# Kernel optimization log

Measured on AMD Instinct MI355X. Metric: run time of the kernel, lower is better.

The kernel has to match this reference:

```python
import jax, jax.numpy as jnp
import numpy as np

N_NODES = 100000
N_EDGES = 1250000
F_RAW = 48      # raw node feature dim
F_LOC = 16      # location embedding dim
F1 = 48         # filters_1
F_OUT = 64      # out_channels


def _glorot(key, shape):
    fan_in, fan_out = shape[0], shape[1]
    scale = jnp.sqrt(6.0 / (fan_in + fan_out)).astype(jnp.float32)
    return jax.random.uniform(key, shape, jnp.float32, -1.0, 1.0) * scale


def setup_inputs() -> dict:
    key = jax.random.key(0)
    k_e, k_x, k_l, k_w1, k_w2 = jax.random.split(key, 5)
    edge_indices = jax.random.randint(k_e, (2, N_EDGES), 0, N_NODES, dtype=jnp.int64)
    features = jax.random.normal(k_x, (N_NODES, F_RAW), jnp.float32)
    location_embedding = jax.random.normal(k_l, (N_NODES, F_LOC), jnp.float32)
    W1 = _glorot(k_w1, (F_RAW + F_LOC, F1))
    b1 = jnp.zeros((F1,), jnp.float32)
    W2 = _glorot(k_w2, (F1 + F_LOC, F_OUT))
    b2 = jnp.zeros((F_OUT,), jnp.float32)
    return {"edge_indices": edge_indices, "features": features,
            "location_embedding": location_embedding,
            "W1": W1, "b1": b1, "W2": W2, "b2": b2}


def gcn_conv(x, src, dst, W, b, n_nodes):
    """PyG GCNConv: add self-loops, symmetric normalization, linear + bias."""
    h = x @ W  # [N, F_out]
    # degree counts include the self-loop (+1)
    deg = jnp.zeros((n_nodes,), h.dtype).at[dst].add(1.0) + 1.0
    dinv = jax.lax.rsqrt(deg)  # deg >= 1 so always finite
    coef = dinv[src] * dinv[dst]  # [E]
    agg = jnp.zeros((n_nodes, h.shape[1]), h.dtype).at[dst].add(h[src] * coef[:, None])
    # self-loop contribution: dinv[i]^2 * h[i]
    return agg + h * (dinv * dinv)[:, None] + b


def reference(edge_indices, features, location_embedding, W1, b1, W2, b2):
    src, dst = edge_indices[0], edge_indices[1]
    n = features.shape[0]
    x = jnp.concatenate([features, location_embedding], axis=-1)
    x = gcn_conv(x, src, dst, W1, b1, n)
    x = jax.nn.relu(x)
    # dropout is identity in eval mode (reference is inference semantics)
    x = jnp.concatenate([x, location_embedding], axis=-1)
    x = gcn_conv(x, src, dst, W2, b2, n)
    return x
```

## Files before the change

kernel.cpp:

```cpp
#include <hip/hip_runtime.h>
#include <hip/hip_fp16.h>

#define N_NODES 100000
#define N_EDGES 1250000
#define F_RAW 48
#define F_LOC 16
#define F1 48
#define F_IN1 64
#define F_IN2 64
#define F_OUT 64

#define NB_BIN 100
#define CHUNK (N_EDGES / NB_BIN)
#define NBUK 391
#define NSCAN (NBUK * NB_BIN)
#define NSCAN_PARTS ((NSCAN + 1023) / 1024)

typedef _Float16 half8_t __attribute__((ext_vector_type(8)));
typedef float floatx4 __attribute__((ext_vector_type(4)));

__global__ void k_detect(const unsigned* edges_u32, int* flag) {
    __shared__ int any;
    if (threadIdx.x == 0) any = 0;
    __syncthreads();
    int nz = 0;
    for (int i = threadIdx.x; i < 2048; i += 256) {
        if (edges_u32[2 * i + 1] != 0u) nz = 1;
    }
    if (nz) atomicOr(&any, 1);
    __syncthreads();
    if (threadIdx.x == 0) *flag = any;
}

__device__ __forceinline__ void load_edge(const void* edges, int is32, int e,
                                          int& s, int& d) {
    if (is32) {
        const int* p = (const int*)edges;
        s = p[e];
        d = p[N_EDGES + e];
    } else {
        const long long* p = (const long long*)edges;
        s = (int)p[e];
        d = (int)p[N_EDGES + e];
    }
}

__global__ __launch_bounds__(1024) void k_prepA(const void* edges,
                                                const int* flag,
                                                int* __restrict__ src32,
                                                int* __restrict__ dst32,
                                                int* __restrict__ bhist) {
    __shared__ int hist[NBUK];
    int b = blockIdx.x, t = threadIdx.x;
    for (int k = t; k < NBUK; k += 1024) hist[k] = 0;
    __syncthreads();
    int is32 = *flag;
    int e0 = b * CHUNK;
    int e1 = e0 + CHUNK;
    for (int e = e0 + t; e < e1; e += 1024) {
        int s, d;
        load_edge(edges, is32, e, s, d);
        src32[e] = s;
        dst32[e] = d;
        atomicAdd(&hist[d >> 8], 1);
    }
    __syncthreads();
    for (int k = t; k < NBUK; k += 1024) bhist[k * NB_BIN + b] = hist[k];
}

__global__ __launch_bounds__(256) void k_gscan_part(const int* __restrict__ in,
                                                    int* __restrict__ part,
                                                    int n) {
    int b = blockIdx.x, t = threadIdx.x;
    int i0 = b * 1024 + t * 4;
    int s = 0;
#pragma unroll
    for (int j = 0; j < 4; ++j) {
        int i = i0 + j;
        if (i < n) s += in[i];
    }
#pragma unroll
    for (int m = 1; m < 64; m <<= 1) s += __shfl_xor(s, m);
    __shared__ int ws[4];
    if ((t & 63) == 0) ws[t >> 6] = s;
    __syncthreads();
    if (t == 0) part[b] = ws[0] + ws[1] + ws[2] + ws[3];
}

__global__ __launch_bounds__(64) void k_gscan_top(int* __restrict__ part,
                                                  int nb) {
    int t = threadIdx.x;
    int v = (t < nb) ? part[t] : 0;
    int x = v;
#pragma unroll
    for (int off = 1; off < 64; off <<= 1) {
        int u = __shfl_up(x, off);
        if (t >= off) x += u;
    }
    if (t < nb) part[t] = x - v;
}

__global__ __launch_bounds__(256) void k_gscan_down(int* __restrict__ data,
                                                    const int* __restrict__ part,
                                                    int n) {
    int b = blockIdx.x, t = threadIdx.x;
    int lane = t & 63, wv = t >> 6;
    int i0 = b * 1024 + t * 4;
    int v[4];
    int s = 0;
#pragma unroll
    for (int j = 0; j < 4; ++j) {
        int i = i0 + j;
        v[j] = (i < n) ? data[i] : 0;
        s += v[j];
    }
    int x = s;
#pragma unroll
    for (int off = 1; off < 64; off <<= 1) {
        int u = __shfl_up(x, off);
        if (lane >= off) x += u;
    }
    __shared__ int ws[4];
    if (lane == 63) ws[wv] = x;
    __syncthreads();
    int woff = 0;
    for (int w = 0; w < wv; ++w) woff += ws[w];
    int run = part[b] + woff + (x - s);
#pragma unroll
    for (int j = 0; j < 4; ++j) {
        int i = i0 + j;
        if (i < n) {
            data[i] = run;
            run += v[j];
        }
    }
}

__global__ __launch_bounds__(1024) void k_place(const int* __restrict__ src32,
                                                const int* __restrict__ dst32,
                                                const int* __restrict__ bhist,
                                                unsigned* __restrict__ binned) {
    __shared__ int cnt[NBUK];
    int b = blockIdx.x, t = threadIdx.x;
    for (int k = t; k < NBUK; k += 1024) cnt[k] = bhist[k * NB_BIN + b];
    __syncthreads();
    int e0 = b * CHUNK;
    int e1 = e0 + CHUNK;
    for (int e = e0 + t; e < e1; e += 1024) {
        int s = src32[e];
        int d = dst32[e];
        int p = atomicAdd(&cnt[d >> 8], 1);
        binned[p] = ((unsigned)(d & 255) << 17) | (unsigned)s;
    }
}

__global__ __launch_bounds__(256) void k_bucket(
    const unsigned* __restrict__ binned, const int* __restrict__ bhist,
    float* __restrict__ dinv, int* __restrict__ rowptr,
    unsigned* __restrict__ csr4) {
    int k = blockIdx.x, t = threadIdx.x;
    int lane = t & 63, wv = t >> 6;
    __shared__ int ldeg[256];
    __shared__ int wcnt[256];
    __shared__ int ws4[4];
    int base = bhist[k * NB_BIN];
    int next = (k + 1 < NBUK) ? bhist[(k + 1) * NB_BIN] : N_EDGES;
    int len = next - base;
    ldeg[t] = 0;
    __syncthreads();
    for (int i = t; i < len; i += 256)
        atomicAdd(&ldeg[binned[base + i] >> 17], 1);
    __syncthreads();
    int degv = ldeg[t];
    int x = degv;
#pragma unroll
    for (int off = 1; off < 64; off <<= 1) {
        int u = __shfl_up(x, off);
        if (lane >= off) x += u;
    }
    if (lane == 63) ws4[wv] = x;
    __syncthreads();
    int woff = 0;
    for (int w = 0; w < wv; ++w) woff += ws4[w];
    int excl = woff + x - degv;
    int node = k * 256 + t;
    if (node < N_NODES) {
        dinv[node] = rsqrtf((float)degv + 1.0f);
        rowptr[node] = base + excl;
    }
    wcnt[t] = base + excl;
    __syncthreads();
    for (int i = t; i < len; i += 256) {
        unsigned ent = binned[base + i];
        int dl = ent >> 17;
        int p = atomicAdd(&wcnt[dl], 1);
        csr4[p] = ent & 0x1FFFFu;
    }
    if (k == 0 && t == 0) rowptr[N_NODES] = N_EDGES;
}

__global__ __launch_bounds__(256) void k_coef(unsigned* __restrict__ csr4,
                                              const float* __restrict__ dinv) {
    int i = blockIdx.x * 256 + threadIdx.x;
    if (i >= N_EDGES / 4) return;
    uint4 v = reinterpret_cast<uint4*>(csr4)[i];
    v.x = (v.x << 14) | (unsigned)__half_as_ushort(__float2half(dinv[v.x]));
    v.y = (v.y << 14) | (unsigned)__half_as_ushort(__float2half(dinv[v.y]));
    v.z = (v.z << 14) | (unsigned)__half_as_ushort(__float2half(dinv[v.z]));
    v.w = (v.w << 14) | (unsigned)__half_as_ushort(__float2half(dinv[v.w]));
    reinterpret_cast<uint4*>(csr4)[i] = v;
}

__global__ __launch_bounds__(256) void k_x0(const float* __restrict__ feat,
                                            const float* __restrict__ loc,
                                            __half* __restrict__ x0) {
    int idx = blockIdx.x * 256 + threadIdx.x;
    if (idx >= N_NODES * 8) return;
    int node = idx >> 3;
    int s = idx & 7;
    const float* srcp = (s < 6) ? feat + (size_t)node * F_RAW + s * 8
                                : loc + (size_t)node * F_LOC + (s - 6) * 8;
    float4 f0 = reinterpret_cast<const float4*>(srcp)[0];
    float4 f1 = reinterpret_cast<const float4*>(srcp)[1];
    __half2 q[4];
    q[0] = __halves2half2(__float2half(f0.x), __float2half(f0.y));
    q[1] = __halves2half2(__float2half(f0.z), __float2half(f0.w));
    q[2] = __halves2half2(__float2half(f1.x), __float2half(f1.y));
    q[3] = __halves2half2(__float2half(f1.z), __float2half(f1.w));
    reinterpret_cast<int4*>(x0)[idx] = *reinterpret_cast<int4*>(q);
}

__global__ void k_wprep(const float* __restrict__ W, __half* __restrict__ Wpk,
                        int M, int CT) {
    int lane = threadIdx.x;
    for (int ct = 0; ct < CT; ++ct)
        for (int kt = 0; kt < 2; ++kt)
            for (int j = 0; j < 8; ++j) {
                int k = kt * 32 + (lane >> 4) * 8 + j;
                int c = ct * 16 + (lane & 15);
                Wpk[((ct * 2 + kt) * 64 + lane) * 8 + j] =
                    __float2half(W[k * M + c]);
            }
}

template <int CT, int ZPAD>
__global__ __launch_bounds__(256) void k_gemm(const __half* __restrict__ X,
                                              const __half* __restrict__ Wpk,
                                              __half* __restrict__ Y) {
    int wid = threadIdx.x >> 6;
    int lane = threadIdx.x & 63;
    int nb = (blockIdx.x * 4 + wid) * 32;
    if (nb >= N_NODES) return;
    half8_t b[CT][2];
#pragma unroll
    for (int ct = 0; ct < CT; ++ct)
#pragma unroll
        for (int kt = 0; kt < 2; ++kt)
            b[ct][kt] =
                *reinterpret_cast<const half8_t*>(Wpk + ((ct * 2 + kt) * 64 + lane) * 8);
    int r = lane & 15;
    int ks = (lane >> 4) * 8;
    half8_t a[2][2];
#pragma unroll
    for (int rt = 0; rt < 2; ++rt)
#pragma unroll
        for (int kt = 0; kt < 2; ++kt)
            a[rt][kt] = *reinterpret_cast<const half8_t*>(
                X + ((size_t)(nb + rt * 16 + r) * 64 + kt * 32 + ks));
    floatx4 acc[2][CT];
#pragma unroll
    for (int rt = 0; rt < 2; ++rt)
#pragma unroll
        for (int ct = 0; ct < CT; ++ct) {
            floatx4 z = {0.f, 0.f, 0.f, 0.f};
            z = __builtin_amdgcn_mfma_f32_16x16x32_f16(a[rt][0], b[ct][0], z, 0, 0, 0);
            z = __builtin_amdgcn_mfma_f32_16x16x32_f16(a[rt][1], b[ct][1], z, 0, 0, 0);
            acc[rt][ct] = z;
        }
    int row0 = (lane >> 4) * 4;
    int col = lane & 15;
#pragma unroll
    for (int rt = 0; rt < 2; ++rt)
#pragma unroll
        for (int ct = 0; ct < CT; ++ct)
#pragma unroll
            for (int j = 0; j < 4; ++j) {
                int node = nb + rt * 16 + row0 + j;
                Y[(size_t)node * 64 + ct * 16 + col] = __float2half(acc[rt][ct][j]);
            }
    if (ZPAD) {
        int node = nb + (lane & 31);
        int slot = 6 + (lane >> 5);
        *reinterpret_cast<int4*>(Y + (size_t)node * 64 + slot * 8) =
            make_int4(0, 0, 0, 0);
    }
}

__device__ __forceinline__ __half2 c2_from(unsigned A) {
    unsigned b = A & 0x3FFFu;
    unsigned p = b | (b << 16);
    return *reinterpret_cast<__half2*>(&p);
}

__device__ __forceinline__ void fma8h(const int4& p, __half2 c2, __half2 a[4]) {
    const __half2* h = reinterpret_cast<const __half2*>(&p);
#pragma unroll
    for (int j = 0; j < 4; ++j) a[j] = __hfma2(h[j], c2, a[j]);
}

__device__ __forceinline__ __half2 shfl_xor_h2(__half2 v, int m) {
    int i = *reinterpret_cast<int*>(&v);
    i = __shfl_xor(i, m);
    return *reinterpret_cast<__half2*>(&i);
}

__global__ __launch_bounds__(256) void k_agg1(
    const __half* __restrict__ h1h, const float* __restrict__ dinv,
    const int* __restrict__ rowptr, const unsigned* __restrict__ csr4,
    const float* __restrict__ loc, const float* __restrict__ b1,
    __half* __restrict__ x1h) {
    int wave = threadIdx.x >> 6;
    int lane = threadIdx.x & 63;
    int grp = lane >> 3;
    int l8 = lane & 7;
    int node = blockIdx.x * 4 + wave;
    if (node >= N_NODES) return;
    int r0 = rowptr[node], r1 = rowptr[node + 1];
    const char* h1c = reinterpret_cast<const char*>(h1h);
    float di = dinv[node];
    int4 hs = *reinterpret_cast<const int4*>(h1c + ((size_t)node << 7) + (l8 << 4));
    int len = r1 - r0;
    int L = (len + 7) >> 3;
    int gs = r0 + grp * L;
    int ge = gs + L;
    if (ge > r1) ge = r1;
    __half2 z2 = __float2half2_rn(0.f);
    __half2 a0[4] = {z2, z2, z2, z2};
    __half2 a1[4] = {z2, z2, z2, z2};
    int e = gs;
    for (; e + 1 < ge; e += 2) {
        unsigned A = csr4[e];
        unsigned B = csr4[e + 1];
        int4 vA = *reinterpret_cast<const int4*>(h1c + ((A >> 14) << 7) + (l8 << 4));
        int4 vB = *reinterpret_cast<const int4*>(h1c + ((B >> 14) << 7) + (l8 << 4));
        fma8h(vA, c2_from(A), a0);
        fma8h(vB, c2_from(B), a1);
    }
    if (e < ge) {
        unsigned A = csr4[e];
        int4 vA = *reinterpret_cast<const int4*>(h1c + ((A >> 14) << 7) + (l8 << 4));
        fma8h(vA, c2_from(A), a0);
    }
#pragma unroll
    for (int j = 0; j < 4; ++j) a0[j] = __hadd2(a0[j], a1[j]);
#pragma unroll
    for (int j = 0; j < 4; ++j) {
        a0[j] = __hadd2(a0[j], shfl_xor_h2(a0[j], 8));
        a0[j] = __hadd2(a0[j], shfl_xor_h2(a0[j], 16));
        a0[j] = __hadd2(a0[j], shfl_xor_h2(a0[j], 32));
    }
    if (lane < 8) {
        __half2 q[4];
        if (l8 < 6) {
            float d2 = di * di;
            const float4* b1v = reinterpret_cast<const float4*>(b1);
            float4 bA = b1v[l8 * 2];
            float4 bB = b1v[l8 * 2 + 1];
            float bb[8] = {bA.x, bA.y, bA.z, bA.w, bB.x, bB.y, bB.z, bB.w};
            const __half2* hh = reinterpret_cast<const __half2*>(&hs);
            float o[8];
#pragma unroll
            for (int j = 0; j < 4; ++j) {
                float2 t = __half22float2(hh[j]);
                float2 ag = __half22float2(a0[j]);
                o[2 * j] = fmaxf(fmaf(ag.x, di, fmaf(t.x, d2, bb[2 * j])), 0.f);
                o[2 * j + 1] =
                    fmaxf(fmaf(ag.y, di, fmaf(t.y, d2, bb[2 * j + 1])), 0.f);
            }
#pragma unroll
            for (int j = 0; j < 4; ++j)
                q[j] = __halves2half2(__float2half(o[2 * j]), __float2half(o[2 * j + 1]));
        } else {
            const float* lp = loc + (size_t)node * F_LOC + (l8 - 6) * 8;
            float4 f0 = reinterpret_cast<const float4*>(lp)[0];
            float4 f1 = reinterpret_cast<const float4*>(lp)[1];
            q[0] = __halves2half2(__float2half(f0.x), __float2half(f0.y));
            q[1] = __halves2half2(__float2half(f0.z), __float2half(f0.w));
            q[2] = __halves2half2(__float2half(f1.x), __float2half(f1.y));
            q[3] = __halves2half2(__float2half(f1.z), __float2half(f1.w));
        }
        reinterpret_cast<int4*>(x1h)[(size_t)node * 8 + l8] =
            *reinterpret_cast<int4*>(q);
    }
}

__global__ __launch_bounds__(256) void k_out(
    const __half* __restrict__ h2h, const float* __restrict__ dinv,
    const int* __restrict__ rowptr, const unsigned* __restrict__ csr4,
    const float* __restrict__ b2, float* __restrict__ out) {
    int wave = threadIdx.x >> 6;
    int lane = threadIdx.x & 63;
    int grp = lane >> 3;
    int l8 = lane & 7;
    int node = blockIdx.x * 4 + wave;
    if (node >= N_NODES) return;
    int r0 = rowptr[node], r1 = rowptr[node + 1];
    const char* h2c = reinterpret_cast<const char*>(h2h);
    float di = dinv[node];
    int4 hs = *reinterpret_cast<const int4*>(h2c + ((size_t)node << 7) + (l8 << 4));
    int len = r1 - r0;
    int L = (len + 7) >> 3;
    int gs = r0 + grp * L;
    int ge = gs + L;
    if (ge > r1) ge = r1;
    __half2 z2 = __float2half2_rn(0.f);
    __half2 a0[4] = {z2, z2, z2, z2};
    __half2 a1[4] = {z2, z2, z2, z2};
    int e = gs;
    for (; e + 1 < ge; e += 2) {
        unsigned A = csr4[e];
        unsigned B = csr4[e + 1];
        int4 vA = *reinterpret_cast<const int4*>(h2c + ((A >> 14) << 7) + (l8 << 4));
        int4 vB = *reinterpret_cast<const int4*>(h2c + ((B >> 14) << 7) + (l8 << 4));
        fma8h(vA, c2_from(A), a0);
        fma8h(vB, c2_from(B), a1);
    }
    if (e < ge) {
        unsigned A = csr4[e];
        int4 vA = *reinterpret_cast<const int4*>(h2c + ((A >> 14) << 7) + (l8 << 4));
        fma8h(vA, c2_from(A), a0);
    }
#pragma unroll
    for (int j = 0; j < 4; ++j) a0[j] = __hadd2(a0[j], a1[j]);
#pragma unroll
    for (int j = 0; j < 4; ++j) {
        a0[j] = __hadd2(a0[j], shfl_xor_h2(a0[j], 8));
        a0[j] = __hadd2(a0[j], shfl_xor_h2(a0[j], 16));
        a0[j] = __hadd2(a0[j], shfl_xor_h2(a0[j], 32));
    }
    if (lane < 8) {
        float d2 = di * di;
        const float4* b2v = reinterpret_cast<const float4*>(b2);
        float4 bA = b2v[l8 * 2];
        float4 bB = b2v[l8 * 2 + 1];
        float bb[8] = {bA.x, bA.y, bA.z, bA.w, bB.x, bB.y, bB.z, bB.w};
        const __half2* hh = reinterpret_cast<const __half2*>(&hs);
        float o[8];
#pragma unroll
        for (int j = 0; j < 4; ++j) {
            float2 t = __half22float2(hh[j]);
            float2 ag = __half22float2(a0[j]);
            o[2 * j] = fmaf(ag.x, di, fmaf(t.x, d2, bb[2 * j]));
            o[2 * j + 1] = fmaf(ag.y, di, fmaf(t.y, d2, bb[2 * j + 1]));
        }
        float4* ov = reinterpret_cast<float4*>(out + (size_t)node * F_OUT);
        ov[l8 * 2] = make_float4(o[0], o[1], o[2], o[3]);
        ov[l8 * 2 + 1] = make_float4(o[4], o[5], o[6], o[7]);
    }
}

extern "C" void kernel_launch(void* const* d_in, const int* in_sizes, int n_in,
                              void* d_out, int out_size, void* d_ws,
                              size_t ws_size, hipStream_t stream) {
    const void* edges = d_in[0];
    const float* feat = (const float*)d_in[1];
    const float* loc = (const float*)d_in[2];
    const float* W1 = (const float*)d_in[3];
    const float* b1 = (const float*)d_in[4];
    const float* W2 = (const float*)d_in[5];
    const float* b2 = (const float*)d_in[6];
    float* out = (float*)d_out;

    char* ws = (char*)d_ws;
    float* dinv = (float*)(ws + 0);
    int* rowptr = (int*)(ws + 400000);
    int* src32 = (int*)(ws + 800016);
    int* dst32 = (int*)(ws + 5800016);
    int* bhist = (int*)(ws + 10800016);
    int* bsum = (int*)(ws + 10956416);
    unsigned* binned = (unsigned*)(ws + 10956672);
    unsigned* csr4 = (unsigned*)(ws + 15956672);
    __half* x0h = (__half*)(ws + 20956672);
    __half* h1h = (__half*)(ws + 33756672);
    __half* h2h = (__half*)(ws + 46556672);
    __half* wpk1 = (__half*)(ws + 59356672);
    __half* wpk2 = (__half*)(ws + 59362816);
    int* flag = (int*)(ws + 59371008);
    __half* x1h = x0h;

    k_detect<<<1, 256, 0, stream>>>((const unsigned*)edges, flag);
    k_wprep<<<1, 64, 0, stream>>>(W1, wpk1, F1, 3);
    k_wprep<<<1, 64, 0, stream>>>(W2, wpk2, F_OUT, 4);
    k_x0<<<(N_NODES * 8 + 255) / 256, 256, 0, stream>>>(feat, loc, x0h);

    k_prepA<<<NB_BIN, 1024, 0, stream>>>(edges, flag, src32, dst32, bhist);
    k_gscan_part<<<NSCAN_PARTS, 256, 0, stream>>>(bhist, bsum, NSCAN);
    k_gscan_top<<<1, 64, 0, stream>>>(bsum, NSCAN_PARTS);
    k_gscan_down<<<NSCAN_PARTS, 256, 0, stream>>>(bhist, bsum, NSCAN);
    k_place<<<NB_BIN, 1024, 0, stream>>>(src32, dst32, bhist, binned);
    k_bucket<<<NBUK, 256, 0, stream>>>(binned, bhist, dinv, rowptr, csr4);
    k_coef<<<(N_EDGES / 4 + 255) / 256, 256, 0, stream>>>(csr4, dinv);

    int gblocks = (N_NODES / 32 + 3) / 4;
    k_gemm<3, 1><<<gblocks, 256, 0, stream>>>(x0h, wpk1, h1h);
    k_agg1<<<(N_NODES + 3) / 4, 256, 0, stream>>>(h1h, dinv, rowptr, csr4,
                                                  loc, b1, x1h);
    k_gemm<4, 0><<<gblocks, 256, 0, stream>>>(x1h, wpk2, h2h);
    k_out<<<(N_NODES + 3) / 4, 256, 0, stream>>>(h2h, dinv, rowptr, csr4, b2,
                                                 out);
}
```

Before: 165.8 us.

## Fuse fp32-to-fp16 input conversion into first GEMM and widen CSR entries

Removes the separate x0 conversion kernel: the first GEMM now reads fp32 features and location embeddings directly and converts them to half in registers. The packed 32-bit CSR entry (source index plus coefficient) becomes an 8-byte entry holding a precomputed byte offset and a duplicated half2 coefficient. This drops the shift and mask work from the aggregation inner loops. The cost is twice the CSR bytes read per edge in both aggregation kernels, and the CSR buffer now reuses the src32/dst32 workspace region.

```diff
diff --git a/kernel.cpp b/kernel.cpp
--- a/kernel.cpp
+++ b/kernel.cpp
@@ -199,35 +199,20 @@
     if (k == 0 && t == 0) rowptr[N_NODES] = N_EDGES;
 }
 
-__global__ __launch_bounds__(256) void k_coef(unsigned* __restrict__ csr4,
-                                              const float* __restrict__ dinv) {
+__global__ __launch_bounds__(256) void k_csr8(const unsigned* __restrict__ csr4,
+                                              const float* __restrict__ dinv,
+                                              int2* __restrict__ csr8) {
     int i = blockIdx.x * 256 + threadIdx.x;
-    if (i >= N_EDGES / 4) return;
-    uint4 v = reinterpret_cast<uint4*>(csr4)[i];
-    v.x = (v.x << 14) | (unsigned)__half_as_ushort(__float2half(dinv[v.x]));
-    v.y = (v.y << 14) | (unsigned)__half_as_ushort(__float2half(dinv[v.y]));
-    v.z = (v.z << 14) | (unsigned)__half_as_ushort(__float2half(dinv[v.z]));
-    v.w = (v.w << 14) | (unsigned)__half_as_ushort(__float2half(dinv[v.w]));
-    reinterpret_cast<uint4*>(csr4)[i] = v;
-}
-
-__global__ __launch_bounds__(256) void k_x0(const float* __restrict__ feat,
-                                            const float* __restrict__ loc,
-                                            __half* __restrict__ x0) {
-    int idx = blockIdx.x * 256 + threadIdx.x;
-    if (idx >= N_NODES * 8) return;
-    int node = idx >> 3;
-    int s = idx & 7;
-    const float* srcp = (s < 6) ? feat + (size_t)node * F_RAW + s * 8
-                                : loc + (size_t)node * F_LOC + (s - 6) * 8;
-    float4 f0 = reinterpret_cast<const float4*>(srcp)[0];
-    float4 f1 = reinterpret_cast<const float4*>(srcp)[1];
-    __half2 q[4];
-    q[0] = __halves2half2(__float2half(f0.x), __float2half(f0.y));
-    q[1] = __halves2half2(__float2half(f0.z), __float2half(f0.w));
-    q[2] = __halves2half2(__float2half(f1.x), __float2half(f1.y));
-    q[3] = __halves2half2(__float2half(f1.z), __float2half(f1.w));
-    reinterpret_cast<int4*>(x0)[idx] = *reinterpret_cast<int4*>(q);
+    if (i >= N_EDGES / 2) return;
+    uint2 v = reinterpret_cast<const uint2*>(csr4)[i];
+    unsigned h0 = (unsigned)__half_as_ushort(__float2half(dinv[v.x]));
+    unsigned h1 = (unsigned)__half_as_ushort(__float2half(dinv[v.y]));
+    int4 o;
+    o.x = (int)(v.x << 7);
+    o.y = (int)(h0 | (h0 << 16));
+    o.z = (int)(v.y << 7);
+    o.w = (int)(h1 | (h1 << 16));
+    reinterpret_cast<int4*>(csr8)[i] = o;
 }
 
 __global__ void k_wprep(const float* __restrict__ W, __half* __restrict__ Wpk,
@@ -243,35 +228,51 @@
             }
 }
 
-template <int CT, int ZPAD>
-__global__ __launch_bounds__(256) void k_gemm(const __half* __restrict__ X,
-                                              const __half* __restrict__ Wpk,
-                                              __half* __restrict__ Y) {
+__global__ __launch_bounds__(256) void k_gemm1(const float* __restrict__ feat,
+                                               const float* __restrict__ loc,
+                                               const __half* __restrict__ Wpk,
+                                               __half* __restrict__ Y) {
     int wid = threadIdx.x >> 6;
     int lane = threadIdx.x & 63;
     int nb = (blockIdx.x * 4 + wid) * 32;
     if (nb >= N_NODES) return;
-    half8_t b[CT][2];
-#pragma unroll
-    for (int ct = 0; ct < CT; ++ct)
+    half8_t b[3][2];
+#pragma unroll
+    for (int ct = 0; ct < 3; ++ct)
 #pragma unroll
         for (int kt = 0; kt < 2; ++kt)
-            b[ct][kt] =
-                *reinterpret_cast<const half8_t*>(Wpk + ((ct * 2 + kt) * 64 + lane) * 8);
+            b[ct][kt] = *reinterpret_cast<const half8_t*>(
+                Wpk + ((ct * 2 + kt) * 64 + lane) * 8);
     int r = lane & 15;
-    int ks = (lane >> 4) * 8;
+    int slot = lane >> 4;
     half8_t a[2][2];
 #pragma unroll
     for (int rt = 0; rt < 2; ++rt)
 #pragma unroll
-        for (int kt = 0; kt < 2; ++kt)
-            a[rt][kt] = *reinterpret_cast<const half8_t*>(
-                X + ((size_t)(nb + rt * 16 + r) * 64 + kt * 32 + ks));
-    floatx4 acc[2][CT];
+        for (int kt = 0; kt < 2; ++kt) {
+            int sl = kt * 4 + slot;
+            int node = nb + rt * 16 + r;
+            const float* sp = (sl < 6)
+                                  ? feat + (size_t)node * F_RAW + sl * 8
+                                  : loc + (size_t)node * F_LOC + (sl - 6) * 8;
+            float4 f0 = reinterpret_cast<const float4*>(sp)[0];
+            float4 f1 = reinterpret_cast<const float4*>(sp)[1];
+            half8_t h;
+            h[0] = (_Float16)f0.x;
+            h[1] = (_Float16)f0.y;
+            h[2] = (_Float16)f0.z;
+            h[3] = (_Float16)f0.w;
+            h[4] = (_Float16)f1.x;
+            h[5] = (_Float16)f1.y;
+            h[6] = (_Float16)f1.z;
+            h[7] = (_Float16)f1.w;
+            a[rt][kt] = h;
+        }
+    floatx4 acc[2][3];
 #pragma unroll
     for (int rt = 0; rt < 2; ++rt)
 #pragma unroll
-        for (int ct = 0; ct < CT; ++ct) {
+        for (int ct = 0; ct < 3; ++ct) {
             floatx4 z = {0.f, 0.f, 0.f, 0.f};
             z = __builtin_amdgcn_mfma_f32_16x16x32_f16(a[rt][0], b[ct][0], z, 0, 0, 0);
             z = __builtin_amdgcn_mfma_f32_16x16x32_f16(a[rt][1], b[ct][1], z, 0, 0, 0);
@@ -282,24 +283,66 @@
 #pragma unroll
     for (int rt = 0; rt < 2; ++rt)
 #pragma unroll
-        for (int ct = 0; ct < CT; ++ct)
+        for (int ct = 0; ct < 3; ++ct)
 #pragma unroll
             for (int j = 0; j < 4; ++j) {
                 int node = nb + rt * 16 + row0 + j;
                 Y[(size_t)node * 64 + ct * 16 + col] = __float2half(acc[rt][ct][j]);
             }
-    if (ZPAD) {
-        int node = nb + (lane & 31);
-        int slot = 6 + (lane >> 5);
-        *reinterpret_cast<int4*>(Y + (size_t)node * 64 + slot * 8) =
-            make_int4(0, 0, 0, 0);
-    }
-}
-
-__device__ __forceinline__ __half2 c2_from(unsigned A) {
-    unsigned b = A & 0x3FFFu;
-    unsigned p = b | (b << 16);
-    return *reinterpret_cast<__half2*>(&p);
+    int node = nb + (lane & 31);
+    int slotp = 6 + (lane >> 5);
+    *reinterpret_cast<int4*>(Y + (size_t)node * 64 + slotp * 8) =
+        make_int4(0, 0, 0, 0);
+}
+
+__global__ __launch_bounds__(256) void k_gemm2(const __half* __restrict__ X,
+                                               const __half* __restrict__ Wpk,
+                                               __half* __restrict__ Y) {
+    int wid = threadIdx.x >> 6;
+    int lane = threadIdx.x & 63;
+    int nb = (blockIdx.x * 4 + wid) * 32;
+    if (nb >= N_NODES) return;
+    half8_t b[4][2];
+#pragma unroll
+    for (int ct = 0; ct < 4; ++ct)
+#pragma unroll
+        for (int kt = 0; kt < 2; ++kt)
+            b[ct][kt] = *reinterpret_cast<const half8_t*>(
+                Wpk + ((ct * 2 + kt) * 64 + lane) * 8);
+    int r = lane & 15;
+    int ks = (lane >> 4) * 8;
+    half8_t a[2][2];
+#pragma unroll
+    for (int rt = 0; rt < 2; ++rt)
+#pragma unroll
+        for (int kt = 0; kt < 2; ++kt)
+            a[rt][kt] = *reinterpret_cast<const half8_t*>(
+                X + ((size_t)(nb + rt * 16 + r) * 64 + kt * 32 + ks));
+    floatx4 acc[2][4];
+#pragma unroll
+    for (int rt = 0; rt < 2; ++rt)
+#pragma unroll
+        for (int ct = 0; ct < 4; ++ct) {
+            floatx4 z = {0.f, 0.f, 0.f, 0.f};
+            z = __builtin_amdgcn_mfma_f32_16x16x32_f16(a[rt][0], b[ct][0], z, 0, 0, 0);
+            z = __builtin_amdgcn_mfma_f32_16x16x32_f16(a[rt][1], b[ct][1], z, 0, 0, 0);
+            acc[rt][ct] = z;
+        }
+    int row0 = (lane >> 4) * 4;
+    int col = lane & 15;
+#pragma unroll
+    for (int rt = 0; rt < 2; ++rt)
+#pragma unroll
+        for (int ct = 0; ct < 4; ++ct)
+#pragma unroll
+            for (int j = 0; j < 4; ++j) {
+                int node = nb + rt * 16 + row0 + j;
+                Y[(size_t)node * 64 + ct * 16 + col] = __float2half(acc[rt][ct][j]);
+            }
+}
+
+__device__ __forceinline__ __half2 h2bits(int y) {
+    return *reinterpret_cast<__half2*>(&y);
 }
 
 __device__ __forceinline__ void fma8h(const int4& p, __half2 c2, __half2 a[4]) {
@@ -316,7 +359,7 @@
 
 __global__ __launch_bounds__(256) void k_agg1(
     const __half* __restrict__ h1h, const float* __restrict__ dinv,
-    const int* __restrict__ rowptr, const unsigned* __restrict__ csr4,
+    const int* __restrict__ rowptr, const int2* __restrict__ csr8,
     const float* __restrict__ loc, const float* __restrict__ b1,
     __half* __restrict__ x1h) {
     int wave = threadIdx.x >> 6;
@@ -326,9 +369,9 @@
     int node = blockIdx.x * 4 + wave;
     if (node >= N_NODES) return;
     int r0 = rowptr[node], r1 = rowptr[node + 1];
-    const char* h1c = reinterpret_cast<const char*>(h1h);
+    const char* h1l = reinterpret_cast<const char*>(h1h) + (l8 << 4);
     float di = dinv[node];
-    int4 hs = *reinterpret_cast<const int4*>(h1c + ((size_t)node << 7) + (l8 << 4));
+    int4 hs = *reinterpret_cast<const int4*>(h1l + ((size_t)node << 7));
     int len = r1 - r0;
     int L = (len + 7) >> 3;
     int gs = r0 + grp * L;
@@ -339,17 +382,17 @@
     __half2 a1[4] = {z2, z2, z2, z2};
     int e = gs;
     for (; e + 1 < ge; e += 2) {
-        unsigned A = csr4[e];
-        unsigned B = csr4[e + 1];
-        int4 vA = *reinterpret_cast<const int4*>(h1c + ((A >> 14) << 7) + (l8 << 4));
-        int4 vB = *reinterpret_cast<const int4*>(h1c + ((B >> 14) << 7) + (l8 << 4));
-        fma8h(vA, c2_from(A), a0);
-        fma8h(vB, c2_from(B), a1);
+        int2 A = csr8[e];
+        int2 B = csr8[e + 1];
+        int4 vA = *reinterpret_cast<const int4*>(h1l + A.x);
+        int4 vB = *reinterpret_cast<const int4*>(h1l + B.x);
+        fma8h(vA, h2bits(A.y), a0);
+        fma8h(vB, h2bits(B.y), a1);
     }
     if (e < ge) {
-        unsigned A = csr4[e];
-        int4 vA = *reinterpret_cast<const int4*>(h1c + ((A >> 14) << 7) + (l8 << 4));
-        fma8h(vA, c2_from(A), a0);
+        int2 A = csr8[e];
+        int4 vA = *reinterpret_cast<const int4*>(h1l + A.x);
+        fma8h(vA, h2bits(A.y), a0);
     }
 #pragma unroll
     for (int j = 0; j < 4; ++j) a0[j] = __hadd2(a0[j], a1[j]);
@@ -379,7 +422,8 @@
             }
 #pragma unroll
             for (int j = 0; j < 4; ++j)
-                q[j] = __halves2half2(__float2half(o[2 * j]), __float2half(o[2 * j + 1]));
+                q[j] = __halves2half2(__float2half(o[2 * j]),
+                                      __float2half(o[2 * j + 1]));
         } else {
             const float* lp = loc + (size_t)node * F_LOC + (l8 - 6) * 8;
             float4 f0 = reinterpret_cast<const float4*>(lp)[0];
@@ -396,7 +440,7 @@
 
 __global__ __launch_bounds__(256) void k_out(
     const __half* __restrict__ h2h, const float* __restrict__ dinv,
-    const int* __restrict__ rowptr, const unsigned* __restrict__ csr4,
+    const int* __restrict__ rowptr, const int2* __restrict__ csr8,
     const float* __restrict__ b2, float* __restrict__ out) {
     int wave = threadIdx.x >> 6;
     int lane = threadIdx.x & 63;
@@ -405,9 +449,9 @@
     int node = blockIdx.x * 4 + wave;
     if (node >= N_NODES) return;
     int r0 = rowptr[node], r1 = rowptr[node + 1];
-    const char* h2c = reinterpret_cast<const char*>(h2h);
+    const char* h2l = reinterpret_cast<const char*>(h2h) + (l8 << 4);
     float di = dinv[node];
-    int4 hs = *reinterpret_cast<const int4*>(h2c + ((size_t)node << 7) + (l8 << 4));
+    int4 hs = *reinterpret_cast<const int4*>(h2l + ((size_t)node << 7));
     int len = r1 - r0;
     int L = (len + 7) >> 3;
     int gs = r0 + grp * L;
@@ -418,17 +462,17 @@
     __half2 a1[4] = {z2, z2, z2, z2};
     int e = gs;
     for (; e + 1 < ge; e += 2) {
-        unsigned A = csr4[e];
-        unsigned B = csr4[e + 1];
-        int4 vA = *reinterpret_cast<const int4*>(h2c + ((A >> 14) << 7) + (l8 << 4));
-        int4 vB = *reinterpret_cast<const int4*>(h2c + ((B >> 14) << 7) + (l8 << 4));
-        fma8h(vA, c2_from(A), a0);
-        fma8h(vB, c2_from(B), a1);
+        int2 A = csr8[e];
+        int2 B = csr8[e + 1];
+        int4 vA = *reinterpret_cast<const int4*>(h2l + A.x);
+        int4 vB = *reinterpret_cast<const int4*>(h2l + B.x);
+        fma8h(vA, h2bits(A.y), a0);
+        fma8h(vB, h2bits(B.y), a1);
     }
     if (e < ge) {
-        unsigned A = csr4[e];
-        int4 vA = *reinterpret_cast<const int4*>(h2c + ((A >> 14) << 7) + (l8 << 4));
-        fma8h(vA, c2_from(A), a0);
+        int2 A = csr8[e];
+        int4 vA = *reinterpret_cast<const int4*>(h2l + A.x);
+        fma8h(vA, h2bits(A.y), a0);
     }
 #pragma unroll
     for (int j = 0; j < 4; ++j) a0[j] = __hadd2(a0[j], a1[j]);
@@ -480,18 +524,17 @@
     int* bsum = (int*)(ws + 10956416);
     unsigned* binned = (unsigned*)(ws + 10956672);
     unsigned* csr4 = (unsigned*)(ws + 15956672);
-    __half* x0h = (__half*)(ws + 20956672);
+    __half* x1h = (__half*)(ws + 20956672);
     __half* h1h = (__half*)(ws + 33756672);
     __half* h2h = (__half*)(ws + 46556672);
     __half* wpk1 = (__half*)(ws + 59356672);
     __half* wpk2 = (__half*)(ws + 59362816);
     int* flag = (int*)(ws + 59371008);
-    __half* x1h = x0h;
+    int2* csr8 = (int2*)(ws + 800016);
 
     k_detect<<<1, 256, 0, stream>>>((const unsigned*)edges, flag);
     k_wprep<<<1, 64, 0, stream>>>(W1, wpk1, F1, 3);
     k_wprep<<<1, 64, 0, stream>>>(W2, wpk2, F_OUT, 4);
-    k_x0<<<(N_NODES * 8 + 255) / 256, 256, 0, stream>>>(feat, loc, x0h);
 
     k_prepA<<<NB_BIN, 1024, 0, stream>>>(edges, flag, src32, dst32, bhist);
     k_gscan_part<<<NSCAN_PARTS, 256, 0, stream>>>(bhist, bsum, NSCAN);
@@ -499,13 +542,13 @@
     k_gscan_down<<<NSCAN_PARTS, 256, 0, stream>>>(bhist, bsum, NSCAN);
     k_place<<<NB_BIN, 1024, 0, stream>>>(src32, dst32, bhist, binned);
     k_bucket<<<NBUK, 256, 0, stream>>>(binned, bhist, dinv, rowptr, csr4);
-    k_coef<<<(N_EDGES / 4 + 255) / 256, 256, 0, stream>>>(csr4, dinv);
+    k_csr8<<<(N_EDGES / 2 + 255) / 256, 256, 0, stream>>>(csr4, dinv, csr8);
 
     int gblocks = (N_NODES / 32 + 3) / 4;
-    k_gemm<3, 1><<<gblocks, 256, 0, stream>>>(x0h, wpk1, h1h);
-    k_agg1<<<(N_NODES + 3) / 4, 256, 0, stream>>>(h1h, dinv, rowptr, csr4,
+    k_gemm1<<<gblocks, 256, 0, stream>>>(feat, loc, wpk1, h1h);
+    k_agg1<<<(N_NODES + 3) / 4, 256, 0, stream>>>(h1h, dinv, rowptr, csr8,
                                                   loc, b1, x1h);
-    k_gemm<4, 0><<<gblocks, 256, 0, stream>>>(x1h, wpk2, h2h);
-    k_out<<<(N_NODES + 3) / 4, 256, 0, stream>>>(h2h, dinv, rowptr, csr4, b2,
+    k_gemm2<<<gblocks, 256, 0, stream>>>(x1h, wpk2, h2h);
+    k_out<<<(N_NODES + 3) / 4, 256, 0, stream>>>(h2h, dinv, rowptr, csr8, b2,
                                                  out);
 }
```

Result: no change. 165.4 us (-0.2%).
